# Performance work log

Hardware: AMD Instinct MI355X
Metric: run time of the kernel (lower is better)

The kernel has to match this reference:

```python
import jax, jax.numpy as jnp
from jax import lax
import numpy as np

BS, L, D, K, R, VOCAB = 4096, 200, 64, 4, 3, 100000
DROP = jnp.float32(-(1 << 31))


def squash(caps):
    # caps: (bs, K, D)
    n = jnp.linalg.norm(caps, axis=2, keepdims=True)   # (bs, K, 1)
    n2 = n * n
    return n2 / ((1.0 + n2) * n + 1e-9) * caps


def setup_inputs() -> dict:
    key = jax.random.key(0)
    ks = jax.random.split(key, 8)
    his = jax.random.randint(ks[0], (BS, L), 0, VOCAB)                     # item ids, 0 = pad
    E = jax.random.normal(ks[1], (VOCAB, D), dtype=jnp.float32)            # itemEmbeds.weight
    S = jax.random.normal(ks[2], (D, D), dtype=jnp.float32)                # bilinear map S
    B0 = jax.random.normal(ks[3], (K, L), dtype=jnp.float32)               # routing logits
    lim1 = 1.0 / np.sqrt(D)
    W1 = jax.random.uniform(ks[4], (D, 4 * D), jnp.float32, -lim1, lim1)   # dense1 (in, out)
    b1 = jax.random.uniform(ks[5], (4 * D,), jnp.float32, -lim1, lim1)
    lim2 = 1.0 / np.sqrt(4 * D)
    W2 = jax.random.uniform(ks[6], (4 * D, D), jnp.float32, -lim2, lim2)   # dense2 (in, out)
    b2 = jax.random.uniform(ks[7], (D,), jnp.float32, -lim2, lim2)
    return {"his": his, "E": E, "S": S, "B0": B0, "W1": W1, "b1": b1, "W2": W2, "b2": b2}


def reference(his, E, S, B0, W1, b1, W2, b2):
    bs = his.shape[0]
    # padding_idx=0 -> embedding row 0 is zero
    E = E.at[0].set(0.0)
    mask = (his != 0)[:, None, :]                       # (bs, 1, L), broadcasts over K
    hisP = jnp.einsum('bld,de->ble', E[his], S)         # (bs, L, D)
    hisPd = lax.stop_gradient(hisP)                     # routing updates run under no_grad
    B = jnp.broadcast_to(lax.stop_gradient(B0)[None], (bs, K, L))
    for _ in range(R - 1):
        W = jax.nn.softmax(jnp.where(mask, B, DROP), axis=2)   # (bs, K, L)
        caps = squash(jnp.einsum('bkl,bld->bkd', W, hisPd))
        B = B + jnp.einsum('bkd,bld->bkl', caps, hisPd)
    W = jax.nn.softmax(jnp.where(mask, B, DROP), axis=2)
    caps = squash(jnp.einsum('bkl,bld->bkd', W, hisP))         # differentiable last iter
    h = jax.nn.relu(jnp.einsum('bkd,df->bkf', caps, W1) + b1)
    return jnp.einsum('bkf,fd->bkd', h, W2) + b2               # (bs, K, D)
```

## Files before the change

kernel.cpp:

```cpp
#include <hip/hip_runtime.h>

#define LSEQ 200
#define KCAP 4
#define NVOC 100000

__global__ __launch_bounds__(256) void precompute_P(
    const float* __restrict__ E, const float* __restrict__ S,
    float* __restrict__ P)
{
    __shared__ __align__(16) float Sl[64 * 64];
    __shared__ __align__(16) float Et[64 * 16];
    const int tid = threadIdx.x;
    #pragma unroll
    for (int t = tid; t < 4096; t += 256) Sl[t] = S[t];
    const int vbase = blockIdx.x * 16;
    #pragma unroll
    for (int t = tid; t < 1024; t += 256) {
        int r = t >> 6, e = t & 63;
        Et[e * 16 + r] = E[(vbase + r) * 64 + e];
    }
    __syncthreads();
    const int d = tid & 63, q = tid >> 6;
    float a0 = 0.f, a1 = 0.f, a2 = 0.f, a3 = 0.f;
    #pragma unroll
    for (int e = 0; e < 64; e++) {
        float4 ev = *(const float4*)(Et + e * 16 + q * 4);
        float  s  = Sl[e * 64 + d];
        a0 = fmaf(ev.x, s, a0);
        a1 = fmaf(ev.y, s, a1);
        a2 = fmaf(ev.z, s, a2);
        a3 = fmaf(ev.w, s, a3);
    }
    const int v0 = vbase + q * 4;
    if (v0 == 0) a0 = 0.f;
    P[(v0 + 0) * 64 + d] = a0;
    P[(v0 + 1) * 64 + d] = a1;
    P[(v0 + 2) * 64 + d] = a2;
    P[(v0 + 3) * 64 + d] = a3;
}

__global__ __launch_bounds__(256, 2) void mind_row(
    const int*   __restrict__ his, const float* __restrict__ P,
    const float* __restrict__ B0,  const float* __restrict__ W1,
    const float* __restrict__ b1,  const float* __restrict__ W2,
    const float* __restrict__ b2,  float* __restrict__ out)
{
    __shared__ __align__(16) float hisPl[LSEQ * 65];
    __shared__ __align__(16) float W4[LSEQ * 4];
    __shared__ __align__(16) float Bm[KCAP * LSEQ];
    __shared__ __align__(16) float caps4[64 * 4];
    __shared__ __align__(16) float part[4 * 4 * 64];
    __shared__ float bigneg[LSEQ];
    __shared__ int   idxs[LSEQ];

    const int b    = blockIdx.x;
    const int tid  = threadIdx.x;
    const int lane = tid & 63;
    const int wv   = tid >> 6;

    for (int l = tid; l < LSEQ; l += 256) {
        int id = his[b * LSEQ + l];
        idxs[l]   = id;
        bigneg[l] = (id != 0) ? 0.f : -1e30f;
    }
    for (int t = tid; t < KCAP * LSEQ; t += 256) Bm[t] = B0[t];
    __syncthreads();

    float hp[50];
    #pragma unroll
    for (int i = 0; i < 50; i++) {
        int l = wv * 50 + i;
        float v = P[idxs[l] * 64 + lane];
        hp[i] = v;
        hisPl[l * 65 + lane] = v;
    }
    __syncthreads();

    for (int r = 0; r < 3; r++) {
        {
            const float* Bk = Bm + wv * LSEQ;
            float x0 = Bk[lane]       + bigneg[lane];
            float x1 = Bk[lane + 64]  + bigneg[lane + 64];
            float x2 = Bk[lane + 128] + bigneg[lane + 128];
            float x3 = (lane < 8) ? (Bk[lane + 192] + bigneg[lane + 192]) : -3.0e38f;
            float m = fmaxf(fmaxf(x0, x1), fmaxf(x2, x3));
            #pragma unroll
            for (int off = 32; off; off >>= 1) m = fmaxf(m, __shfl_xor(m, off, 64));
            float e0 = __expf(x0 - m), e1 = __expf(x1 - m), e2 = __expf(x2 - m);
            float e3 = (lane < 8) ? __expf(x3 - m) : 0.f;
            float s = e0 + e1 + e2 + e3;
            #pragma unroll
            for (int off = 32; off; off >>= 1) s += __shfl_xor(s, off, 64);
            float inv = 1.f / s;
            W4[lane * 4 + wv]         = e0 * inv;
            W4[(lane + 64) * 4 + wv]  = e1 * inv;
            W4[(lane + 128) * 4 + wv] = e2 * inv;
            if (lane < 8) W4[(lane + 192) * 4 + wv] = e3 * inv;
        }
        __syncthreads();

        {
            float a0 = 0, a1 = 0, a2 = 0, a3 = 0;
            #pragma unroll
            for (int i = 0; i < 50; i++) {
                int l = wv * 50 + i;
                float4 w = *(const float4*)(W4 + l * 4);
                float  v = hp[i];
                a0 = fmaf(w.x, v, a0);
                a1 = fmaf(w.y, v, a1);
                a2 = fmaf(w.z, v, a2);
                a3 = fmaf(w.w, v, a3);
            }
            part[wv * 256 + lane]       = a0;
            part[wv * 256 + 64 + lane]  = a1;
            part[wv * 256 + 128 + lane] = a2;
            part[wv * 256 + 192 + lane] = a3;
        }
        __syncthreads();

        {
            float c = part[wv * 64 + lane]       + part[256 + wv * 64 + lane]
                    + part[512 + wv * 64 + lane] + part[768 + wv * 64 + lane];
            float n2 = c * c;
            #pragma unroll
            for (int off = 32; off; off >>= 1) n2 += __shfl_xor(n2, off, 64);
            float n  = sqrtf(n2);
            float sc = n2 / ((1.f + n2) * n + 1e-9f);
            c *= sc;
            caps4[lane * 4 + wv] = c;
        }
        __syncthreads();

        if (r < 2) {
            if (tid < LSEQ) {
                const int l = tid;
                float d0 = 0, d1 = 0, d2 = 0, d3 = 0;
                #pragma unroll 8
                for (int d = 0; d < 64; d++) {
                    float  v = hisPl[l * 65 + d];
                    float4 c = *(const float4*)(caps4 + d * 4);
                    d0 = fmaf(c.x, v, d0);
                    d1 = fmaf(c.y, v, d1);
                    d2 = fmaf(c.z, v, d2);
                    d3 = fmaf(c.w, v, d3);
                }
                Bm[l]       += d0;
                Bm[200 + l] += d1;
                Bm[400 + l] += d2;
                Bm[600 + l] += d3;
            }
            __syncthreads();
        }
    }

    float* h4 = hisPl;
    {
        const int f = tid;
        float h0 = 0, h1 = 0, h2 = 0, h3 = 0;
        #pragma unroll 8
        for (int d = 0; d < 64; d++) {
            float  w = W1[d * 256 + f];
            float4 c = *(const float4*)(caps4 + d * 4);
            h0 = fmaf(c.x, w, h0);
            h1 = fmaf(c.y, w, h1);
            h2 = fmaf(c.z, w, h2);
            h3 = fmaf(c.w, w, h3);
        }
        float bb = b1[f];
        h0 = fmaxf(h0 + bb, 0.f);
        h1 = fmaxf(h1 + bb, 0.f);
        h2 = fmaxf(h2 + bb, 0.f);
        h3 = fmaxf(h3 + bb, 0.f);
        h4[f * 4 + 0] = h0; h4[f * 4 + 1] = h1;
        h4[f * 4 + 2] = h2; h4[f * 4 + 3] = h3;
    }
    __syncthreads();
    {
        float o0 = 0, o1 = 0, o2 = 0, o3 = 0;
        #pragma unroll 8
        for (int i = 0; i < 64; i++) {
            int f = wv * 64 + i;
            float  w  = W2[f * 64 + lane];
            float4 hv = *(const float4*)(h4 + f * 4);
            o0 = fmaf(hv.x, w, o0);
            o1 = fmaf(hv.y, w, o1);
            o2 = fmaf(hv.z, w, o2);
            o3 = fmaf(hv.w, w, o3);
        }
        part[wv * 256 + lane]       = o0;
        part[wv * 256 + 64 + lane]  = o1;
        part[wv * 256 + 128 + lane] = o2;
        part[wv * 256 + 192 + lane] = o3;
    }
    __syncthreads();
    {
        float o = part[wv * 64 + lane]       + part[256 + wv * 64 + lane]
                + part[512 + wv * 64 + lane] + part[768 + wv * 64 + lane];
        out[b * 256 + tid] = o + b2[lane];
    }
}

extern "C" void kernel_launch(void* const* d_in, const int* in_sizes, int n_in,
                              void* d_out, int out_size, void* d_ws, size_t ws_size,
                              hipStream_t stream) {
    const int*   his = (const int*)  d_in[0];
    const float* E   = (const float*)d_in[1];
    const float* S   = (const float*)d_in[2];
    const float* B0  = (const float*)d_in[3];
    const float* W1  = (const float*)d_in[4];
    const float* b1  = (const float*)d_in[5];
    const float* W2  = (const float*)d_in[6];
    const float* b2  = (const float*)d_in[7];
    float* out = (float*)d_out;
    float* P   = (float*)d_ws;

    precompute_P<<<NVOC / 16, 256, 0, stream>>>(E, S, P);
    mind_row<<<4096, 256, 0, stream>>>(his, P, B0, W1, b1, W2, b2, out);
}
```

Baseline: 240.1 us.

## Vectorize P precompute per-row and use float4 gathers and layouts in routing

precompute_P now has each thread compute one full vocabulary row with 64 register accumulators, broadcasting S rows from shared memory as float4, in place of a 16-row tile per block. mind_row gathers P rows as float4 (16 lanes per row, 4 rows per wave instruction) into a padded float4 shared layout. The weighted-sum step gains cross-lane shuffle reductions, and the B-update dot products become float4 with a transposed caps copy. This aims to cut gather and LDS instruction counts, at the cost of more registers and extra shuffles.

```diff
diff --git a/kernel.cpp b/kernel.cpp
--- a/kernel.cpp
+++ b/kernel.cpp
@@ -3,40 +3,50 @@
 #define LSEQ 200
 #define KCAP 4
 #define NVOC 100000
+
+__device__ __forceinline__ void fma4(float4& a, float s, const float4& v) {
+    a.x = fmaf(s, v.x, a.x); a.y = fmaf(s, v.y, a.y);
+    a.z = fmaf(s, v.z, a.z); a.w = fmaf(s, v.w, a.w);
+}
 
 __global__ __launch_bounds__(256) void precompute_P(
     const float* __restrict__ E, const float* __restrict__ S,
     float* __restrict__ P)
 {
-    __shared__ __align__(16) float Sl[64 * 64];
-    __shared__ __align__(16) float Et[64 * 16];
+    __shared__ __align__(16) float4 Sl4[1024];
     const int tid = threadIdx.x;
     #pragma unroll
-    for (int t = tid; t < 4096; t += 256) Sl[t] = S[t];
-    const int vbase = blockIdx.x * 16;
+    for (int t = tid; t < 1024; t += 256) Sl4[t] = ((const float4*)S)[t];
+    __syncthreads();
+
+    const int v = blockIdx.x * 256 + tid;
+    const bool ok = (v < NVOC);
+    const float4* __restrict__ Er = (const float4*)E + (size_t)(ok ? v : 0) * 16;
+
+    float4 acc[16];
     #pragma unroll
-    for (int t = tid; t < 1024; t += 256) {
-        int r = t >> 6, e = t & 63;
-        Et[e * 16 + r] = E[(vbase + r) * 64 + e];
-    }
-    __syncthreads();
-    const int d = tid & 63, q = tid >> 6;
-    float a0 = 0.f, a1 = 0.f, a2 = 0.f, a3 = 0.f;
-    #pragma unroll
-    for (int e = 0; e < 64; e++) {
-        float4 ev = *(const float4*)(Et + e * 16 + q * 4);
-        float  s  = Sl[e * 64 + d];
-        a0 = fmaf(ev.x, s, a0);
-        a1 = fmaf(ev.y, s, a1);
-        a2 = fmaf(ev.z, s, a2);
-        a3 = fmaf(ev.w, s, a3);
-    }
-    const int v0 = vbase + q * 4;
-    if (v0 == 0) a0 = 0.f;
-    P[(v0 + 0) * 64 + d] = a0;
-    P[(v0 + 1) * 64 + d] = a1;
-    P[(v0 + 2) * 64 + d] = a2;
-    P[(v0 + 3) * 64 + d] = a3;
+    for (int j = 0; j < 16; j++) acc[j] = make_float4(0.f, 0.f, 0.f, 0.f);
+
+    #pragma unroll 1
+    for (int ec = 0; ec < 16; ec += 2) {
+        float4 ea = Er[ec], eb = Er[ec + 1];
+        float ev[8] = {ea.x, ea.y, ea.z, ea.w, eb.x, eb.y, eb.z, eb.w};
+        #pragma unroll
+        for (int e = 0; e < 8; e++) {
+            const float4* Srow = Sl4 + (ec * 4 + e) * 16;
+            #pragma unroll
+            for (int j = 0; j < 16; j++) fma4(acc[j], ev[e], Srow[j]);
+        }
+    }
+    if (ok) {
+        float4* Pr = (float4*)P + (size_t)v * 16;
+        if (v == 0) {
+            #pragma unroll
+            for (int j = 0; j < 16; j++) acc[j] = make_float4(0.f, 0.f, 0.f, 0.f);
+        }
+        #pragma unroll
+        for (int j = 0; j < 16; j++) Pr[j] = acc[j];
+    }
 }
 
 __global__ __launch_bounds__(256, 2) void mind_row(
@@ -45,18 +55,18 @@
     const float* __restrict__ b1,  const float* __restrict__ W2,
     const float* __restrict__ b2,  float* __restrict__ out)
 {
-    __shared__ __align__(16) float hisPl[LSEQ * 65];
-    __shared__ __align__(16) float W4[LSEQ * 4];
-    __shared__ __align__(16) float Bm[KCAP * LSEQ];
-    __shared__ __align__(16) float caps4[64 * 4];
-    __shared__ __align__(16) float part[4 * 4 * 64];
+    __shared__ __align__(16) float4 hisP4[LSEQ * 17];
+    __shared__ __align__(16) float  W4[LSEQ * 4];
+    __shared__ __align__(16) float  Bm[KCAP * LSEQ];
+    __shared__ __align__(16) float  caps4[64 * 4];
+    __shared__ __align__(16) float4 capsT4[KCAP * 16];
+    __shared__ __align__(16) float4 part4[16 * 17];
     __shared__ float bigneg[LSEQ];
     __shared__ int   idxs[LSEQ];
 
-    const int b    = blockIdx.x;
-    const int tid  = threadIdx.x;
-    const int lane = tid & 63;
-    const int wv   = tid >> 6;
+    const int b = blockIdx.x, tid = threadIdx.x;
+    const int lane = tid & 63, wv = tid >> 6;
+    const int q = lane >> 4, r = lane & 15;
 
     for (int l = tid; l < LSEQ; l += 256) {
         int id = his[b * LSEQ + l];
@@ -66,17 +76,21 @@
     for (int t = tid; t < KCAP * LSEQ; t += 256) Bm[t] = B0[t];
     __syncthreads();
 
-    float hp[50];
+    float4 hp4[13];
+    const float4* P4 = (const float4*)P;
     #pragma unroll
-    for (int i = 0; i < 50; i++) {
-        int l = wv * 50 + i;
-        float v = P[idxs[l] * 64 + lane];
-        hp[i] = v;
-        hisPl[l * 65 + lane] = v;
-    }
-    __syncthreads();
-
-    for (int r = 0; r < 3; r++) {
+    for (int i = 0; i < 13; i++) {
+        int  l     = wv * 50 + i * 4 + q;
+        bool valid = (i < 12) || (q < 2);
+        int  lc    = valid ? l : 0;
+        float4 vv  = P4[(size_t)idxs[lc] * 16 + r];
+        if (!valid) vv = make_float4(0.f, 0.f, 0.f, 0.f);
+        hp4[i] = vv;
+        if (valid) hisP4[l * 17 + r] = vv;
+    }
+    __syncthreads();
+
+    for (int rr = 0; rr < 3; rr++) {
         {
             const float* Bk = Bm + wv * LSEQ;
             float x0 = Bk[lane]       + bigneg[lane];
@@ -100,60 +114,74 @@
         __syncthreads();
 
         {
-            float a0 = 0, a1 = 0, a2 = 0, a3 = 0;
-            #pragma unroll
-            for (int i = 0; i < 50; i++) {
-                int l = wv * 50 + i;
-                float4 w = *(const float4*)(W4 + l * 4);
-                float  v = hp[i];
-                a0 = fmaf(w.x, v, a0);
-                a1 = fmaf(w.y, v, a1);
-                a2 = fmaf(w.z, v, a2);
-                a3 = fmaf(w.w, v, a3);
-            }
-            part[wv * 256 + lane]       = a0;
-            part[wv * 256 + 64 + lane]  = a1;
-            part[wv * 256 + 128 + lane] = a2;
-            part[wv * 256 + 192 + lane] = a3;
+            float4 a0 = make_float4(0,0,0,0), a1 = a0, a2 = a0, a3 = a0;
+            #pragma unroll
+            for (int i = 0; i < 13; i++) {
+                int l  = wv * 50 + i * 4 + q;
+                int lc = (l < LSEQ - 1) ? l : (LSEQ - 1);
+                float4 w = *(const float4*)(W4 + lc * 4);
+                fma4(a0, w.x, hp4[i]); fma4(a1, w.y, hp4[i]);
+                fma4(a2, w.z, hp4[i]); fma4(a3, w.w, hp4[i]);
+            }
+            #pragma unroll
+            for (int off = 16; off <= 32; off <<= 1) {
+                a0.x += __shfl_xor(a0.x, off, 64); a0.y += __shfl_xor(a0.y, off, 64);
+                a0.z += __shfl_xor(a0.z, off, 64); a0.w += __shfl_xor(a0.w, off, 64);
+                a1.x += __shfl_xor(a1.x, off, 64); a1.y += __shfl_xor(a1.y, off, 64);
+                a1.z += __shfl_xor(a1.z, off, 64); a1.w += __shfl_xor(a1.w, off, 64);
+                a2.x += __shfl_xor(a2.x, off, 64); a2.y += __shfl_xor(a2.y, off, 64);
+                a2.z += __shfl_xor(a2.z, off, 64); a2.w += __shfl_xor(a2.w, off, 64);
+                a3.x += __shfl_xor(a3.x, off, 64); a3.y += __shfl_xor(a3.y, off, 64);
+                a3.z += __shfl_xor(a3.z, off, 64); a3.w += __shfl_xor(a3.w, off, 64);
+            }
+            if (q == 0) {
+                part4[(wv * 4 + 0) * 17 + r] = a0;
+                part4[(wv * 4 + 1) * 17 + r] = a1;
+                part4[(wv * 4 + 2) * 17 + r] = a2;
+                part4[(wv * 4 + 3) * 17 + r] = a3;
+            }
         }
         __syncthreads();
 
         {
-            float c = part[wv * 64 + lane]       + part[256 + wv * 64 + lane]
-                    + part[512 + wv * 64 + lane] + part[768 + wv * 64 + lane];
+            const float* pf = (const float*)part4;
+            float c = pf[(0 * 4 + wv) * 68 + lane] + pf[(1 * 4 + wv) * 68 + lane]
+                    + pf[(2 * 4 + wv) * 68 + lane] + pf[(3 * 4 + wv) * 68 + lane];
             float n2 = c * c;
             #pragma unroll
             for (int off = 32; off; off >>= 1) n2 += __shfl_xor(n2, off, 64);
             float n  = sqrtf(n2);
             float sc = n2 / ((1.f + n2) * n + 1e-9f);
             c *= sc;
-            caps4[lane * 4 + wv] = c;
+            caps4[lane * 4 + wv]          = c;
+            ((float*)capsT4)[wv * 64 + lane] = c;
         }
         __syncthreads();
 
-        if (r < 2) {
+        if (rr < 2) {
             if (tid < LSEQ) {
                 const int l = tid;
-                float d0 = 0, d1 = 0, d2 = 0, d3 = 0;
-                #pragma unroll 8
-                for (int d = 0; d < 64; d++) {
-                    float  v = hisPl[l * 65 + d];
-                    float4 c = *(const float4*)(caps4 + d * 4);
-                    d0 = fmaf(c.x, v, d0);
-                    d1 = fmaf(c.y, v, d1);
-                    d2 = fmaf(c.z, v, d2);
-                    d3 = fmaf(c.w, v, d3);
+                float s0 = 0, s1 = 0, s2 = 0, s3 = 0;
+                #pragma unroll
+                for (int j = 0; j < 16; j++) {
+                    float4 h  = hisP4[l * 17 + j];
+                    float4 c0 = capsT4[j],      c1 = capsT4[16 + j];
+                    float4 c2 = capsT4[32 + j], c3 = capsT4[48 + j];
+                    s0 = fmaf(h.x, c0.x, fmaf(h.y, c0.y, fmaf(h.z, c0.z, fmaf(h.w, c0.w, s0))));
+                    s1 = fmaf(h.x, c1.x, fmaf(h.y, c1.y, fmaf(h.z, c1.z, fmaf(h.w, c1.w, s1))));
+                    s2 = fmaf(h.x, c2.x, fmaf(h.y, c2.y, fmaf(h.z, c2.z, fmaf(h.w, c2.w, s2))));
+                    s3 = fmaf(h.x, c3.x, fmaf(h.y, c3.y, fmaf(h.z, c3.z, fmaf(h.w, c3.w, s3))));
                 }
-                Bm[l]       += d0;
-                Bm[200 + l] += d1;
-                Bm[400 + l] += d2;
-                Bm[600 + l] += d3;
+                Bm[l]       += s0;
+                Bm[200 + l] += s1;
+                Bm[400 + l] += s2;
+                Bm[600 + l] += s3;
             }
             __syncthreads();
         }
     }
 
-    float* h4 = hisPl;
+    float4* h44 = (float4*)hisP4;
     {
         const int f = tid;
         float h0 = 0, h1 = 0, h2 = 0, h3 = 0;
@@ -161,41 +189,34 @@
         for (int d = 0; d < 64; d++) {
             float  w = W1[d * 256 + f];
             float4 c = *(const float4*)(caps4 + d * 4);
-            h0 = fmaf(c.x, w, h0);
-            h1 = fmaf(c.y, w, h1);
-            h2 = fmaf(c.z, w, h2);
-            h3 = fmaf(c.w, w, h3);
+            h0 = fmaf(c.x, w, h0); h1 = fmaf(c.y, w, h1);
+            h2 = fmaf(c.z, w, h2); h3 = fmaf(c.w, w, h3);
         }
         float bb = b1[f];
-        h0 = fmaxf(h0 + bb, 0.f);
-        h1 = fmaxf(h1 + bb, 0.f);
-        h2 = fmaxf(h2 + bb, 0.f);
-        h3 = fmaxf(h3 + bb, 0.f);
-        h4[f * 4 + 0] = h0; h4[f * 4 + 1] = h1;
-        h4[f * 4 + 2] = h2; h4[f * 4 + 3] = h3;
-    }
-    __syncthreads();
+        h44[f] = make_float4(fmaxf(h0 + bb, 0.f), fmaxf(h1 + bb, 0.f),
+                             fmaxf(h2 + bb, 0.f), fmaxf(h3 + bb, 0.f));
+    }
+    __syncthreads();
+    float* partf = (float*)part4;
     {
         float o0 = 0, o1 = 0, o2 = 0, o3 = 0;
         #pragma unroll 8
         for (int i = 0; i < 64; i++) {
             int f = wv * 64 + i;
             float  w  = W2[f * 64 + lane];
-            float4 hv = *(const float4*)(h4 + f * 4);
-            o0 = fmaf(hv.x, w, o0);
-            o1 = fmaf(hv.y, w, o1);
-            o2 = fmaf(hv.z, w, o2);
-            o3 = fmaf(hv.w, w, o3);
-        }
-        part[wv * 256 + lane]       = o0;
-        part[wv * 256 + 64 + lane]  = o1;
-        part[wv * 256 + 128 + lane] = o2;
-        part[wv * 256 + 192 + lane] = o3;
+            float4 hv = h44[f];
+            o0 = fmaf(hv.x, w, o0); o1 = fmaf(hv.y, w, o1);
+            o2 = fmaf(hv.z, w, o2); o3 = fmaf(hv.w, w, o3);
+        }
+        partf[wv * 256 + lane]       = o0;
+        partf[wv * 256 + 64 + lane]  = o1;
+        partf[wv * 256 + 128 + lane] = o2;
+        partf[wv * 256 + 192 + lane] = o3;
     }
     __syncthreads();
     {
-        float o = part[wv * 64 + lane]       + part[256 + wv * 64 + lane]
-                + part[512 + wv * 64 + lane] + part[768 + wv * 64 + lane];
+        float o = partf[wv * 64 + lane]       + partf[256 + wv * 64 + lane]
+                + partf[512 + wv * 64 + lane] + partf[768 + wv * 64 + lane];
         out[b * 256 + tid] = o + b2[lane];
     }
 }
@@ -214,6 +235,6 @@
     float* out = (float*)d_out;
     float* P   = (float*)d_ws;
 
-    precompute_P<<<NVOC / 16, 256, 0, stream>>>(E, S, P);
+    precompute_P<<<(NVOC + 255) / 256, 256, 0, stream>>>(E, S, P);
     mind_row<<<4096, 256, 0, stream>>>(his, P, B0, W1, b1, W2, b2, out);
 }
```

Result: slower. 256.3 us (+6.7%).
